# Performance work log

Measured on AMD Instinct MI355X. Metric: run time of the kernel, lower is better.

The kernel has to match this reference:

```python
import jax, jax.numpy as jnp
import numpy as np

NUM_TOKENS = 16384
DIM = 4096
N_EXPERTS = 256
ROUTE_SCALE = 1.0


def setup_inputs() -> dict:
    key = jax.random.key(0)
    k_x, k_w = jax.random.split(key)
    x = jax.random.normal(k_x, (NUM_TOKENS, DIM), dtype=jnp.float32)
    # nn.init.normal_(weight, std=0.02)
    weight = 0.02 * jax.random.normal(k_w, (N_EXPERTS, DIM), dtype=jnp.float32)
    return {"x": x, "weight": weight}


def reference(x, weight):
    # Router GEMM: [T, D] @ [D, E] -> [T, E]
    scores = jnp.einsum("td,ed->te", x, weight)
    # Eval-mode token_choice path: softmax in fp32
    probs = jax.nn.softmax(scores.astype(jnp.float32), axis=-1)  # [T, E]
    indices = jnp.argmax(probs, axis=-1, keepdims=True)  # [T, 1] int
    # Hard one-hot scatter of argmax
    y_hard = jax.nn.one_hot(indices[:, 0], N_EXPERTS, dtype=probs.dtype)  # [T, E]
    # Straight-through estimator mix
    ste = jax.lax.stop_gradient(y_hard - probs) + probs
    # Gather routing weight at the selected expert
    weights = jnp.take_along_axis(ste, indices, axis=-1)  # [T, 1]
    weights = (weights * ROUTE_SCALE).astype(x.dtype)
    return weights, indices
```

## Files before the change

### kernel.cpp

```cpp
#include <hip/hip_runtime.h>
#include <stdint.h>

#define NUM_TOKENS 16384
#define DIM        4096
#define NEXP       256
#define MB         64
#define BK         64
#define KHALF      2048
#define NITER      (KHALF / BK)
#define APAD       72
#define MARGIN     0.025f
#define CAP        16384

typedef __attribute__((ext_vector_type(4))) float   f32x4;
typedef __attribute__((ext_vector_type(8))) __bf16  bf16x8;
typedef __attribute__((ext_vector_type(8))) unsigned short u16x8;

static __device__ __forceinline__ unsigned short f32_to_bf16(float f) {
    unsigned int u = __float_as_uint(f);
    u += 0x7fffu + ((u >> 16) & 1u);
    return (unsigned short)(u >> 16);
}

__global__ void cvt_weights(const float* __restrict__ w,
                            unsigned short* __restrict__ wh,
                            int* __restrict__ counter) {
    if (blockIdx.x == 0 && threadIdx.x == 0) *counter = 0;
    const int n4 = NEXP * DIM / 4;
    const int stride = gridDim.x * blockDim.x;
    for (int i = blockIdx.x * blockDim.x + threadIdx.x; i < n4; i += stride) {
        float4 v = ((const float4*)w)[i];
        ushort4 h;
        h.x = f32_to_bf16(v.x); h.y = f32_to_bf16(v.y);
        h.z = f32_to_bf16(v.z); h.w = f32_to_bf16(v.w);
        ((ushort4*)wh)[i] = h;
    }
}

__global__ __launch_bounds__(256, 3) void gate_main(
    const float* __restrict__ x,
    const unsigned short* __restrict__ wh,
    float* __restrict__ ps)
{
    __shared__ unsigned short lAh[MB][APAD];
    __shared__ unsigned short lBh[NEXP * BK];

    const int tid  = threadIdx.x;
    const int wv   = tid >> 6;
    const int lane = tid & 63;
    const int tile = blockIdx.x >> 1;
    const int half = blockIdx.x & 1;
    const int tok0 = tile * MB;
    const int kbase = half * KHALF;

    const int ta   = tid >> 2;
    const int kseg = (tid & 3) * 16;
    const float* xrow = x + (size_t)(tok0 + ta) * DIM + kbase + kseg;

    const int esub   = lane >> 3;
    const int bk_off = ((lane & 7) ^ esub) * 8;

    const int quad = lane >> 4;
    const int col  = lane & 15;

    f32x4 acc[4][4];
    #pragma unroll
    for (int mt = 0; mt < 4; ++mt)
        #pragma unroll
        for (int nt = 0; nt < 4; ++nt)
            acc[mt][nt] = f32x4{0.f, 0.f, 0.f, 0.f};

    float4 xv0 = *(const float4*)(xrow);
    float4 xv1 = *(const float4*)(xrow + 4);
    float4 xv2 = *(const float4*)(xrow + 8);
    float4 xv3 = *(const float4*)(xrow + 12);

    for (int it = 0; it < NITER; ++it) {
        const int k0 = it * BK;

        #pragma unroll
        for (int jj = 0; jj < 8; ++jj) {
            const int e = wv * 64 + jj * 8 + esub;
            const unsigned short* gh = wh + (size_t)e * DIM + kbase + k0 + bk_off;
            unsigned short* dh = &lBh[(wv * 64 + jj * 8) * BK];
            __builtin_amdgcn_global_load_lds(
                (const __attribute__((address_space(1))) unsigned int*)gh,
                (__attribute__((address_space(3))) unsigned int*)dh, 16, 0, 0);
        }

        {
            u16x8 h0, h1;
            h0[0] = f32_to_bf16(xv0.x); h0[1] = f32_to_bf16(xv0.y);
            h0[2] = f32_to_bf16(xv0.z); h0[3] = f32_to_bf16(xv0.w);
            h0[4] = f32_to_bf16(xv1.x); h0[5] = f32_to_bf16(xv1.y);
            h0[6] = f32_to_bf16(xv1.z); h0[7] = f32_to_bf16(xv1.w);
            h1[0] = f32_to_bf16(xv2.x); h1[1] = f32_to_bf16(xv2.y);
            h1[2] = f32_to_bf16(xv2.z); h1[3] = f32_to_bf16(xv2.w);
            h1[4] = f32_to_bf16(xv3.x); h1[5] = f32_to_bf16(xv3.y);
            h1[6] = f32_to_bf16(xv3.z); h1[7] = f32_to_bf16(xv3.w);
            *(u16x8*)&lAh[ta][kseg]     = h0;
            *(u16x8*)&lAh[ta][kseg + 8] = h1;
        }
        __syncthreads();

        if (it + 1 < NITER) {
            xv0 = *(const float4*)(xrow + (it + 1) * BK);
            xv1 = *(const float4*)(xrow + (it + 1) * BK + 4);
            xv2 = *(const float4*)(xrow + (it + 1) * BK + 8);
            xv3 = *(const float4*)(xrow + (it + 1) * BK + 12);
        }

        #pragma unroll
        for (int kk = 0; kk < BK; kk += 32) {
            const int kc = kk >> 3;
            bf16x8 ah[4], bh[4];
            #pragma unroll
            for (int mt = 0; mt < 4; ++mt)
                ah[mt] = *(const bf16x8*)&lAh[mt * 16 + col][kk + quad * 8];
            #pragma unroll
            for (int nt = 0; nt < 4; ++nt) {
                const int e = wv * 64 + nt * 16 + col;
                const int cpos = (((kc + quad) ^ (col & 7)) * 8);
                bh[nt] = *(const bf16x8*)&lBh[e * BK + cpos];
            }
            #pragma unroll
            for (int mt = 0; mt < 4; ++mt)
                #pragma unroll
                for (int nt = 0; nt < 4; ++nt)
                    acc[mt][nt] = __builtin_amdgcn_mfma_f32_16x16x32_bf16(
                        ah[mt], bh[nt], acc[mt][nt], 0, 0, 0);
        }
        __syncthreads();
    }

    float* base = ps + ((size_t)half * NUM_TOKENS + tok0) * NEXP;
    #pragma unroll
    for (int mt = 0; mt < 4; ++mt)
        #pragma unroll
        for (int r = 0; r < 4; ++r) {
            const int tok = mt * 16 + quad * 4 + r;
            #pragma unroll
            for (int nt = 0; nt < 4; ++nt)
                base[(size_t)tok * NEXP + wv * 64 + nt * 16 + col] = acc[mt][nt][r];
        }
}

__global__ void reduce_top2(const float* __restrict__ ps,
                            float* __restrict__ out,
                            int* __restrict__ counter,
                            int4* __restrict__ entries) {
    const int gw   = (blockIdx.x * blockDim.x + threadIdx.x) >> 6;
    const int lane = threadIdx.x & 63;
    const int nw   = (gridDim.x * blockDim.x) >> 6;
    for (int t = gw; t < NUM_TOKENS; t += nw) {
        const float4 a = *(const float4*)(ps + (size_t)t * NEXP + lane * 4);
        const float4 b = *(const float4*)(ps + ((size_t)NUM_TOKENS + t) * NEXP + lane * 4);
        float s[4] = {a.x + b.x, a.y + b.y, a.z + b.z, a.w + b.w};
        float t1s = s[0]; int t1e = lane * 4;
        float t2s = s[1]; int t2e = lane * 4 + 1;
        if (t2s > t1s) { float ts = t1s; int te = t1e; t1s = t2s; t1e = t2e; t2s = ts; t2e = te; }
        #pragma unroll
        for (int j = 2; j < 4; ++j) {
            if (s[j] > t1s)      { t2s = t1s; t2e = t1e; t1s = s[j]; t1e = lane * 4 + j; }
            else if (s[j] > t2s) { t2s = s[j]; t2e = lane * 4 + j; }
        }
        #pragma unroll
        for (int m = 1; m <= 32; m <<= 1) {
            float o1s = __shfl_xor(t1s, m); int o1e = __shfl_xor(t1e, m);
            float o2s = __shfl_xor(t2s, m); int o2e = __shfl_xor(t2e, m);
            bool o1_top = (o1s > t1s) || (o1s == t1s && o1e < t1e);
            if (o1_top) {
                bool keep_t1 = (t1s > o2s) || (t1s == o2s && t1e < o2e);
                t2s = keep_t1 ? t1s : o2s; t2e = keep_t1 ? t1e : o2e;
                t1s = o1s; t1e = o1e;
            } else {
                bool o1_2nd = (o1s > t2s) || (o1s == t2s && o1e < t2e);
                if (o1_2nd) { t2s = o1s; t2e = o1e; }
            }
        }
        if (lane == 0) {
            out[t] = 1.0f;
            out[NUM_TOKENS + t] = (float)t1e;
            if (t1s - t2s < MARGIN) {
                int slot = atomicAdd(counter, 1);
                if (slot < CAP) entries[slot] = make_int4(t, t1e, t2e, 0);
            }
        }
    }
}

__global__ void refine(const float* __restrict__ x,
                       const float* __restrict__ w,
                       const int* __restrict__ counter,
                       const int4* __restrict__ entries,
                       float* __restrict__ out) {
    const int gwave  = (blockIdx.x * blockDim.x + threadIdx.x) >> 6;
    const int lane   = threadIdx.x & 63;
    const int nwaves = (gridDim.x * blockDim.x) >> 6;
    int n = *counter; if (n > CAP) n = CAP;
    for (int i = gwave; i < n; i += nwaves) {
        int4 e = entries[i];
        const float* xr = x + (size_t)e.x * DIM;
        const float* w1 = w + (size_t)e.y * DIM;
        const float* w2 = w + (size_t)e.z * DIM;
        double d1 = 0.0, d2 = 0.0;
        for (int k = lane; k < DIM; k += 64) {
            double xv = (double)xr[k];
            d1 += xv * (double)w1[k];
            d2 += xv * (double)w2[k];
        }
        #pragma unroll
        for (int m = 32; m > 0; m >>= 1) {
            d1 += __shfl_xor(d1, m);
            d2 += __shfl_xor(d2, m);
        }
        if (lane == 0) {
            int best = (d1 > d2) ? e.y : ((d2 > d1) ? e.z : (e.y < e.z ? e.y : e.z));
            out[NUM_TOKENS + e.x] = (float)best;
        }
    }
}

extern "C" void kernel_launch(void* const* d_in, const int* in_sizes, int n_in,
                              void* d_out, int out_size, void* d_ws, size_t ws_size,
                              hipStream_t stream) {
    const float* x = (const float*)d_in[0];
    const float* w = (const float*)d_in[1];
    float* out = (float*)d_out;

    char* ws = (char*)d_ws;
    unsigned short* wh = (unsigned short*)ws;
    int*  counter = (int*)(ws + (2u << 20));
    int4* entries = (int4*)(ws + (2u << 20) + 16);
    float* ps     = (float*)(ws + (4u << 20));

    cvt_weights<<<256, 256, 0, stream>>>(w, wh, counter);
    gate_main<<<2 * NUM_TOKENS / MB, 256, 0, stream>>>(x, wh, ps);
    reduce_top2<<<512, 256, 0, stream>>>(ps, out, counter, entries);
    refine<<<256, 256, 0, stream>>>(x, w, counter, entries, out);
}
```

Baseline: 435.4 us.

## Fuse top-2 selection into GEMM epilogue and drop split-K partial scores

The router GEMM no longer splits K in two and writes partial score matrices to workspace. Each block now handles 32 tokens over the full K range and computes the top-2 experts in registers, using wave shuffles and a small shared-memory cross-wave merge. This removes the 32 MB round trip of partial scores and the separate reduce kernel launch. In exchange, the grid stays at 512 blocks but each block does twice as many K iterations with a smaller M tile, so weight reuse per LDS load is halved.

```diff
diff --git a/kernel.cpp b/kernel.cpp
--- a/kernel.cpp
+++ b/kernel.cpp
@@ -4,11 +4,11 @@
 #define NUM_TOKENS 16384
 #define DIM        4096
 #define NEXP       256
-#define MB         64
+#define MB         32
 #define BK         64
-#define KHALF      2048
-#define NITER      (KHALF / BK)
+#define NITER      (DIM / BK)
 #define APAD       72
+#define NWAVES     4
 #define MARGIN     0.025f
 #define CAP        16384
 
@@ -37,25 +37,25 @@
     }
 }
 
-__global__ __launch_bounds__(256, 3) void gate_main(
+__global__ __launch_bounds__(256, 4) void gate_main(
     const float* __restrict__ x,
     const unsigned short* __restrict__ wh,
-    float* __restrict__ ps)
+    float* __restrict__ out,
+    int* __restrict__ counter,
+    int4* __restrict__ entries)
 {
     __shared__ unsigned short lAh[MB][APAD];
     __shared__ unsigned short lBh[NEXP * BK];
+    __shared__ float4 cand[NWAVES][MB];
 
     const int tid  = threadIdx.x;
     const int wv   = tid >> 6;
     const int lane = tid & 63;
-    const int tile = blockIdx.x >> 1;
-    const int half = blockIdx.x & 1;
-    const int tok0 = tile * MB;
-    const int kbase = half * KHALF;
-
-    const int ta   = tid >> 2;
-    const int kseg = (tid & 3) * 16;
-    const float* xrow = x + (size_t)(tok0 + ta) * DIM + kbase + kseg;
+    const int tok0 = blockIdx.x * MB;
+
+    const int ta   = tid >> 3;
+    const int kseg = (tid & 7) * 8;
+    const float* xrow = x + (size_t)(tok0 + ta) * DIM + kseg;
 
     const int esub   = lane >> 3;
     const int bk_off = ((lane & 7) ^ esub) * 8;
@@ -63,17 +63,15 @@
     const int quad = lane >> 4;
     const int col  = lane & 15;
 
-    f32x4 acc[4][4];
+    f32x4 acc[2][4];
     #pragma unroll
-    for (int mt = 0; mt < 4; ++mt)
+    for (int mt = 0; mt < 2; ++mt)
         #pragma unroll
         for (int nt = 0; nt < 4; ++nt)
             acc[mt][nt] = f32x4{0.f, 0.f, 0.f, 0.f};
 
     float4 xv0 = *(const float4*)(xrow);
     float4 xv1 = *(const float4*)(xrow + 4);
-    float4 xv2 = *(const float4*)(xrow + 8);
-    float4 xv3 = *(const float4*)(xrow + 12);
 
     for (int it = 0; it < NITER; ++it) {
         const int k0 = it * BK;
@@ -81,7 +79,7 @@
         #pragma unroll
         for (int jj = 0; jj < 8; ++jj) {
             const int e = wv * 64 + jj * 8 + esub;
-            const unsigned short* gh = wh + (size_t)e * DIM + kbase + k0 + bk_off;
+            const unsigned short* gh = wh + (size_t)e * DIM + k0 + bk_off;
             unsigned short* dh = &lBh[(wv * 64 + jj * 8) * BK];
             __builtin_amdgcn_global_load_lds(
                 (const __attribute__((address_space(1))) unsigned int*)gh,
@@ -89,33 +87,26 @@
         }
 
         {
-            u16x8 h0, h1;
+            u16x8 h0;
             h0[0] = f32_to_bf16(xv0.x); h0[1] = f32_to_bf16(xv0.y);
             h0[2] = f32_to_bf16(xv0.z); h0[3] = f32_to_bf16(xv0.w);
             h0[4] = f32_to_bf16(xv1.x); h0[5] = f32_to_bf16(xv1.y);
             h0[6] = f32_to_bf16(xv1.z); h0[7] = f32_to_bf16(xv1.w);
-            h1[0] = f32_to_bf16(xv2.x); h1[1] = f32_to_bf16(xv2.y);
-            h1[2] = f32_to_bf16(xv2.z); h1[3] = f32_to_bf16(xv2.w);
-            h1[4] = f32_to_bf16(xv3.x); h1[5] = f32_to_bf16(xv3.y);
-            h1[6] = f32_to_bf16(xv3.z); h1[7] = f32_to_bf16(xv3.w);
-            *(u16x8*)&lAh[ta][kseg]     = h0;
-            *(u16x8*)&lAh[ta][kseg + 8] = h1;
+            *(u16x8*)&lAh[ta][kseg] = h0;
         }
         __syncthreads();
 
         if (it + 1 < NITER) {
             xv0 = *(const float4*)(xrow + (it + 1) * BK);
             xv1 = *(const float4*)(xrow + (it + 1) * BK + 4);
-            xv2 = *(const float4*)(xrow + (it + 1) * BK + 8);
-            xv3 = *(const float4*)(xrow + (it + 1) * BK + 12);
         }
 
         #pragma unroll
         for (int kk = 0; kk < BK; kk += 32) {
             const int kc = kk >> 3;
-            bf16x8 ah[4], bh[4];
-            #pragma unroll
-            for (int mt = 0; mt < 4; ++mt)
+            bf16x8 ah[2], bh[4];
+            #pragma unroll
+            for (int mt = 0; mt < 2; ++mt)
                 ah[mt] = *(const bf16x8*)&lAh[mt * 16 + col][kk + quad * 8];
             #pragma unroll
             for (int nt = 0; nt < 4; ++nt) {
@@ -124,7 +115,7 @@
                 bh[nt] = *(const bf16x8*)&lBh[e * BK + cpos];
             }
             #pragma unroll
-            for (int mt = 0; mt < 4; ++mt)
+            for (int mt = 0; mt < 2; ++mt)
                 #pragma unroll
                 for (int nt = 0; nt < 4; ++nt)
                     acc[mt][nt] = __builtin_amdgcn_mfma_f32_16x16x32_bf16(
@@ -133,41 +124,50 @@
         __syncthreads();
     }
 
-    float* base = ps + ((size_t)half * NUM_TOKENS + tok0) * NEXP;
     #pragma unroll
-    for (int mt = 0; mt < 4; ++mt)
+    for (int mt = 0; mt < 2; ++mt) {
         #pragma unroll
         for (int r = 0; r < 4; ++r) {
-            const int tok = mt * 16 + quad * 4 + r;
-            #pragma unroll
-            for (int nt = 0; nt < 4; ++nt)
-                base[(size_t)tok * NEXP + wv * 64 + nt * 16 + col] = acc[mt][nt][r];
-        }
-}
-
-__global__ void reduce_top2(const float* __restrict__ ps,
-                            float* __restrict__ out,
-                            int* __restrict__ counter,
-                            int4* __restrict__ entries) {
-    const int gw   = (blockIdx.x * blockDim.x + threadIdx.x) >> 6;
-    const int lane = threadIdx.x & 63;
-    const int nw   = (gridDim.x * blockDim.x) >> 6;
-    for (int t = gw; t < NUM_TOKENS; t += nw) {
-        const float4 a = *(const float4*)(ps + (size_t)t * NEXP + lane * 4);
-        const float4 b = *(const float4*)(ps + ((size_t)NUM_TOKENS + t) * NEXP + lane * 4);
-        float s[4] = {a.x + b.x, a.y + b.y, a.z + b.z, a.w + b.w};
-        float t1s = s[0]; int t1e = lane * 4;
-        float t2s = s[1]; int t2e = lane * 4 + 1;
-        if (t2s > t1s) { float ts = t1s; int te = t1e; t1s = t2s; t1e = t2e; t2s = ts; t2e = te; }
-        #pragma unroll
-        for (int j = 2; j < 4; ++j) {
-            if (s[j] > t1s)      { t2s = t1s; t2e = t1e; t1s = s[j]; t1e = lane * 4 + j; }
-            else if (s[j] > t2s) { t2s = s[j]; t2e = lane * 4 + j; }
-        }
-        #pragma unroll
-        for (int m = 1; m <= 32; m <<= 1) {
-            float o1s = __shfl_xor(t1s, m); int o1e = __shfl_xor(t1e, m);
-            float o2s = __shfl_xor(t2s, m); int o2e = __shfl_xor(t2e, m);
+            float t1s = acc[mt][0][r]; int t1e = wv * 64 + col;
+            float t2s = acc[mt][1][r]; int t2e = t1e + 16;
+            if (t2s > t1s) { float ts = t1s; int te = t1e; t1s = t2s; t1e = t2e; t2s = ts; t2e = te; }
+            #pragma unroll
+            for (int nt = 2; nt < 4; ++nt) {
+                float s = acc[mt][nt][r]; int e = wv * 64 + nt * 16 + col;
+                if (s > t1s)      { t2s = t1s; t2e = t1e; t1s = s; t1e = e; }
+                else if (s > t2s) { t2s = s; t2e = e; }
+            }
+            #pragma unroll
+            for (int m = 1; m <= 8; m <<= 1) {
+                float o1s = __shfl_xor(t1s, m); int o1e = __shfl_xor(t1e, m);
+                float o2s = __shfl_xor(t2s, m); int o2e = __shfl_xor(t2e, m);
+                bool o1_top = (o1s > t1s) || (o1s == t1s && o1e < t1e);
+                if (o1_top) {
+                    bool keep_t1 = (t1s > o2s) || (t1s == o2s && t1e < o2e);
+                    t2s = keep_t1 ? t1s : o2s; t2e = keep_t1 ? t1e : o2e;
+                    t1s = o1s; t1e = o1e;
+                } else {
+                    bool o1_2nd = (o1s > t2s) || (o1s == t2s && o1e < t2e);
+                    if (o1_2nd) { t2s = o1s; t2e = o1e; }
+                }
+            }
+            if (col == 0) {
+                int tok = mt * 16 + quad * 4 + r;
+                cand[wv][tok] = make_float4(t1s, __int_as_float(t1e), t2s, __int_as_float(t2e));
+            }
+        }
+    }
+    __syncthreads();
+
+    if (tid < MB) {
+        float4 c0 = cand[0][tid];
+        float t1s = c0.x; int t1e = __float_as_int(c0.y);
+        float t2s = c0.z; int t2e = __float_as_int(c0.w);
+        #pragma unroll
+        for (int wvi = 1; wvi < NWAVES; ++wvi) {
+            float4 c = cand[wvi][tid];
+            float o1s = c.x; int o1e = __float_as_int(c.y);
+            float o2s = c.z; int o2e = __float_as_int(c.w);
             bool o1_top = (o1s > t1s) || (o1s == t1s && o1e < t1e);
             if (o1_top) {
                 bool keep_t1 = (t1s > o2s) || (t1s == o2s && t1e < o2e);
@@ -178,13 +178,12 @@
                 if (o1_2nd) { t2s = o1s; t2e = o1e; }
             }
         }
-        if (lane == 0) {
-            out[t] = 1.0f;
-            out[NUM_TOKENS + t] = (float)t1e;
-            if (t1s - t2s < MARGIN) {
-                int slot = atomicAdd(counter, 1);
-                if (slot < CAP) entries[slot] = make_int4(t, t1e, t2e, 0);
-            }
+        const int gtok = tok0 + tid;
+        out[gtok] = 1.0f;
+        out[NUM_TOKENS + gtok] = (float)t1e;
+        if (t1s - t2s < MARGIN) {
+            int slot = atomicAdd(counter, 1);
+            if (slot < CAP) entries[slot] = make_int4(gtok, t1e, t2e, 0);
         }
     }
 }
@@ -232,10 +231,8 @@
     unsigned short* wh = (unsigned short*)ws;
     int*  counter = (int*)(ws + (2u << 20));
     int4* entries = (int4*)(ws + (2u << 20) + 16);
-    float* ps     = (float*)(ws + (4u << 20));
 
     cvt_weights<<<256, 256, 0, stream>>>(w, wh, counter);
-    gate_main<<<2 * NUM_TOKENS / MB, 256, 0, stream>>>(x, wh, ps);
-    reduce_top2<<<512, 256, 0, stream>>>(ps, out, counter, entries);
+    gate_main<<<NUM_TOKENS / MB, 256, 0, stream>>>(x, wh, out, counter, entries);
     refine<<<256, 256, 0, stream>>>(x, w, counter, entries, out);
 }
```

New measurement: 437.4 us. About the same (+0.5%).
